# Optimization experiments

Hardware: AMD Instinct MI355X
Metric: run time of the kernel (lower is better)

The kernel has to match this reference:

```python
import jax, jax.numpy as jnp
import numpy as np


def setup_inputs() -> dict:
    key = jax.random.key(0)
    ks = jax.random.split(key, 12)
    B, T, S, D, A, E, L, V = 32, 64, 64, 1024, 512, 256, 1024, 12000
    s = 0.02  # weight scale for numerical stability
    return {
        "targets": jax.random.randint(ks[0], (B, T), 0, V),
        "options": jax.random.normal(ks[1], (B, S, D), jnp.float32),
        "h0": jax.random.normal(ks[2], (B, L), jnp.float32),
        "c0": jnp.zeros((B, L), jnp.float32),
        "emb": jax.random.normal(ks[3], (V, E), jnp.float32) * s,
        "W1": jax.random.normal(ks[4], (L, A), jnp.float32) * s,
        "b1": jnp.zeros((A,), jnp.float32),
        "W2": jax.random.normal(ks[5], (D, A), jnp.float32) * s,
        "b2": jnp.zeros((A,), jnp.float32),
        "Va": jax.random.normal(ks[6], (A, 1), jnp.float32) * s,
        "bVa": jnp.zeros((1,), jnp.float32),
        "Wx": jax.random.normal(ks[7], (D + E, 4 * L), jnp.float32) * s,
        "Wh": jax.random.normal(ks[8], (L, 4 * L), jnp.float32) * s,
        "bl": jnp.zeros((4 * L,), jnp.float32),
        "Wd": jax.random.normal(ks[9], (L, V), jnp.float32) * s,
        "bd": jnp.zeros((V,), jnp.float32),
    }


def reference(targets, options, h0, c0, emb, W1, b1, W2, b2, Va, bVa,
              Wx, Wh, bl, Wd, bd):
    L = h0.shape[-1]
    # W2(options) is step-invariant: hoist out of recurrent loop. [B,S,A]
    opt_proj = jnp.einsum('bsd,da->bsa', options, W2) + b2

    def step(carry, x_ids):
        h, c = carry
        # Bahdanau attention: score = V(tanh(W1(h) + W2(options)))
        score = jnp.tanh(h @ W1 + b1)[:, None, :] + opt_proj        # [B,S,A]
        score = jnp.einsum('bsa,ao->bso', score, Va) + bVa          # [B,S,1]
        w = jax.nn.softmax(score, axis=1)                           # [B,S,1]
        context = jnp.sum(w * options, axis=1)                      # [B,D]
        x = jnp.concatenate([context, emb[x_ids]], axis=-1)         # [B,D+E]
        # Keras LSTM cell, gate order i, f, g, o
        z = x @ Wx + h @ Wh + bl                                    # [B,4L]
        i, f, g, o = jnp.split(z, 4, axis=-1)
        c = jax.nn.sigmoid(f) * c + jax.nn.sigmoid(i) * jnp.tanh(g)
        h = jax.nn.sigmoid(o) * jnp.tanh(c)
        probs = jax.nn.softmax(h @ Wd + bd, axis=-1)                # [B,V]
        return (h, c), (probs, w[..., 0])

    (h, c), (out, attn) = jax.lax.scan(step, (h0, c0), targets.T)
    output = jnp.transpose(out, (1, 0, 2))   # [B,T,V]
    attention = attn[-1][..., None]          # last-step attention weights [B,S,1]
    return output, h, c, attention
```

## Files before the change

kernel.cpp:

```cpp
#include <hip/hip_runtime.h>
#include <math.h>


typedef _Float16 fp16;
typedef __attribute__((ext_vector_type(8))) _Float16 fp16x8;
typedef __attribute__((ext_vector_type(4))) _Float16 fp16x4;
typedef __attribute__((ext_vector_type(4))) float f32x4;

constexpr int B = 32, T = 64, S = 64, D = 1024, A = 512, E = 256, L = 1024, V = 12000;
constexpr int G = 4096;
constexpr size_t N_PROBS = (size_t)B * T * V;

__device__ inline void load_lds16(const void* g, void* l) {
  __builtin_amdgcn_global_load_lds(
      (const __attribute__((address_space(1))) unsigned int*)g,
      (__attribute__((address_space(3))) unsigned int*)l, 16, 0, 0);
}


__global__ void k_v2(const float* __restrict__ W2, const float* __restrict__ Va,
                     float* __restrict__ v2) {
  int gw = (blockIdx.x * blockDim.x + threadIdx.x) >> 6;
  int lane = threadIdx.x & 63;
  if (gw >= D) return;
  float acc = 0.f;
  for (int a = lane; a < A; a += 64) acc += W2[(size_t)gw * A + a] * Va[a];
  #pragma unroll
  for (int off = 32; off; off >>= 1) acc += __shfl_down(acc, off);
  if (lane == 0) v2[gw] = acc;
}

__global__ void k_score(const float* __restrict__ options, const float* __restrict__ v2,
                        float* __restrict__ w) {
  int row = (blockIdx.x * blockDim.x + threadIdx.x) >> 6;
  int lane = threadIdx.x & 63;
  if (row >= B * S) return;
  const float* orow = options + (size_t)row * D;
  float acc = 0.f;
  for (int d = lane; d < D; d += 64) acc += orow[d] * v2[d];
  #pragma unroll
  for (int off = 32; off; off >>= 1) acc += __shfl_down(acc, off);
  if (lane == 0) w[row] = acc;
}

__global__ __launch_bounds__(256) void k_attnctx(
    const float* __restrict__ options, const float* __restrict__ wat,
    float* __restrict__ oattn, float* __restrict__ ctx) {
  __shared__ float sw[64];
  const int b = blockIdx.x, tid = threadIdx.x;
  if (tid < 64) {
    float v = wat[b * 64 + tid];
    float m = v;
    #pragma unroll
    for (int off = 32; off; off >>= 1) m = fmaxf(m, __shfl_xor(m, off));
    float e = expf(v - m);
    float s = e;
    #pragma unroll
    for (int off = 32; off; off >>= 1) s += __shfl_xor(s, off);
    float res = e / s;
    sw[tid] = res;
    oattn[b * 64 + tid] = res;
  }
  __syncthreads();
  for (int d = tid; d < D; d += 256) {
    float acc = 0.f;
    #pragma unroll 8
    for (int s = 0; s < 64; ++s)
      acc += sw[s] * options[((size_t)(b * 64 + s)) * D + d];
    ctx[b * D + d] = acc;
  }
}

__global__ __launch_bounds__(256) void k_cx_part(
    const float* __restrict__ ctx, const float* __restrict__ Wx,
    float* __restrict__ cxp) {
  const int jt = blockIdx.x & 15;
  const int bg = (blockIdx.x >> 4) & 3;
  const int kc = blockIdx.x >> 6;
  const int j = jt * 256 + threadIdx.x;
  const int b0 = bg * 8, d0 = kc * 128;
  float acc[8];
  #pragma unroll
  for (int bb = 0; bb < 8; ++bb) acc[bb] = 0.f;
  for (int d = 0; d < 128; ++d) {
    float wv = Wx[(size_t)(d0 + d) * G + j];
    #pragma unroll
    for (int bb = 0; bb < 8; ++bb)
      acc[bb] = fmaf(ctx[(b0 + bb) * D + d0 + d], wv, acc[bb]);
  }
  #pragma unroll
  for (int bb = 0; bb < 8; ++bb)
    cxp[((size_t)kc * 32 + b0 + bb) * G + j] = acc[bb];
}

__global__ void k_cx_reduce(const float* __restrict__ cxp, const float* __restrict__ bl,
                            float* __restrict__ cx) {
  int i = blockIdx.x * 256 + threadIdx.x;
  float s = bl[i & 4095];
  #pragma unroll
  for (int kc = 0; kc < 8; ++kc) s += cxp[(size_t)kc * 131072 + i];
  cx[i] = s;
}

__global__ __launch_bounds__(256) void k_xform(
    const int* __restrict__ targets, const float* __restrict__ emb,
    const float* __restrict__ Wx, const float* __restrict__ Wh,
    const float* __restrict__ h0, const float* __restrict__ c0,
    fp16* __restrict__ eg, fp16* __restrict__ wx2t16, fp16* __restrict__ whp,
    fp16* __restrict__ h16, float* __restrict__ cst) {
  __shared__ float s[64][65];
  const int bid = blockIdx.x;
  const int tid = threadIdx.x;

  if (bid < 2048) {
    int tok = targets[bid];
    eg[(size_t)bid * E + tid] = (fp16)emb[(size_t)tok * E + tid];
    return;
  }
  if (bid < 2304) {
    const int lb = bid - 2048;
    const int et = lb >> 6, jt = lb & 63;
    const int e0 = et * 64, j0 = jt * 64;
    const int jj = tid & 63;
    #pragma unroll
    for (int k = 0; k < 16; ++k) {
      int ee = k * 4 + (tid >> 6);
      s[ee][jj] = Wx[(size_t)(D + e0 + ee) * G + j0 + jj];
    }
    __syncthreads();
    const int jc = tid >> 2, eq = tid & 3;
    fp16x8 o0, o1;
    #pragma unroll
    for (int i = 0; i < 8; ++i) {
      o0[i] = (fp16)s[eq * 16 + i][jc];
      o1[i] = (fp16)s[eq * 16 + 8 + i][jc];
    }
    size_t dst = (size_t)(j0 + jc) * E + e0 + eq * 16;
    *(fp16x8*)(wx2t16 + dst) = o0;
    *(fp16x8*)(wx2t16 + dst + 8) = o1;
    return;
  }
  if (bid < 3328) {
    const int lb = bid - 2304;
    const int lt = lb & 15, ct = lb >> 4;
    const int l0 = lt * 64, c0 = ct * 64;
    const int cc = tid & 63;
    #pragma unroll
    for (int k = 0; k < 16; ++k) {
      int ll = k * 4 + (tid >> 6);
      s[ll][cc] = Wh[(size_t)(l0 + ll) * G + c0 + cc];
    }
    __syncthreads();
    const int c = tid >> 2, lq = tid & 3;
    const int col = c0 + c, g = col >> 10, jj = col & 1023;
    const int rowp = ((jj >> 2) << 4) + (g << 2) + (jj & 3);
    fp16x8 o0, o1;
    #pragma unroll
    for (int i = 0; i < 8; ++i) {
      o0[i] = (fp16)s[lq * 16 + i][c];
      o1[i] = (fp16)s[lq * 16 + 8 + i][c];
    }
    size_t dst = (size_t)rowp * L + l0 + lq * 16;
    *(fp16x8*)(whp + dst) = o0;
    *(fp16x8*)(whp + dst + 8) = o1;
    return;
  }
  {
    const int lb = bid - 3328;
    int i = lb * 256 + tid;
    h16[i] = (fp16)h0[i];
    cst[i] = c0[i];
  }
}

__global__ __launch_bounds__(256) void k_pre_mfma(
    const fp16* __restrict__ Ag, const fp16* __restrict__ Bg,
    const float* __restrict__ cx, fp16* __restrict__ prep) {
  __shared__ __align__(16) char lds[32768];
  char* sA = lds;
  char* sB = lds + 16384;
  const int bid = blockIdx.x;
  const int swz = (bid & 7) * 64 + (bid >> 3);
  const int mt = swz >> 5, nt = swz & 31;
  const int m0 = mt * 128, n0 = nt * 128;
  const int tid = threadIdx.x, w = tid >> 6, lane = tid & 63;
  const int wr = w >> 1, wc = w & 1;

  f32x4 acc[4][4];
  #pragma unroll
  for (int i = 0; i < 4; ++i)
    #pragma unroll
    for (int j = 0; j < 4; ++j) acc[i][j] = (f32x4){0.f, 0.f, 0.f, 0.f};

  int rowc[4], sloc[4];
  #pragma unroll
  for (int i = 0; i < 4; ++i) {
    int c = i * 4 + w;
    rowc[i] = c * 8 + (lane >> 3);
    sloc[i] = (lane & 7) ^ (rowc[i] & 7);
  }

  for (int kk = 0; kk < 4; ++kk) {
    if (kk) __syncthreads();
    const char* ga = (const char*)Ag + kk * 128;
    const char* gb = (const char*)Bg + kk * 128;
    #pragma unroll
    for (int i = 0; i < 4; ++i) {
      int c = i * 4 + w;
      load_lds16(ga + (size_t)(m0 + rowc[i]) * 512 + sloc[i] * 16, sA + c * 1024);
      load_lds16(gb + (size_t)(n0 + rowc[i]) * 512 + sloc[i] * 16, sB + c * 1024);
    }
    __syncthreads();
    #pragma unroll
    for (int ks = 0; ks < 2; ++ks) {
      fp16x8 av[4], bv[4];
      #pragma unroll
      for (int f = 0; f < 4; ++f) {
        int ra = wr * 64 + f * 16 + (lane & 15);
        int ca = (ks * 4 + (lane >> 4)) ^ (ra & 7);
        av[f] = *(const fp16x8*)(sA + ra * 128 + ca * 16);
        int rb = wc * 64 + f * 16 + (lane & 15);
        int cb = (ks * 4 + (lane >> 4)) ^ (rb & 7);
        bv[f] = *(const fp16x8*)(sB + rb * 128 + cb * 16);
      }
      #pragma unroll
      for (int fm = 0; fm < 4; ++fm)
        #pragma unroll
        for (int fn = 0; fn < 4; ++fn)
          acc[fm][fn] = __builtin_amdgcn_mfma_f32_16x16x32_f16(
              av[fm], bv[fn], acc[fm][fn], 0, 0, 0);
    }
  }

  const int r0o = m0 + wr * 64 + ((lane >> 4) << 2);
  const int c0o = n0 + wc * 64 + (lane & 15);
  #pragma unroll
  for (int fn = 0; fn < 4; ++fn) {
    int colg = c0o + fn * 16;
    int g = colg >> 10, jj = colg & 1023;
    int jb = jj >> 2, jo = jj & 3;
    #pragma unroll
    for (int fm = 0; fm < 4; ++fm) {
      #pragma unroll
      for (int r = 0; r < 4; ++r) {
        int row = r0o + fm * 16 + r;
        int b = row >> 6, t = row & 63;
        float v = acc[fm][fn][r] + cx[(size_t)b * G + colg];
        prep[(((size_t)t * 256 + jb) * 32 + b) * 16 + jo * 4 + g] = (fp16)v;
      }
    }
  }
}

__global__ __launch_bounds__(512) void k_step4(
    const fp16* __restrict__ Whp, const fp16* __restrict__ prep,
    const fp16* __restrict__ hin, fp16* __restrict__ hout,
    float* __restrict__ cst, fp16* __restrict__ Hb16,
    float* __restrict__ out_h, float* __restrict__ out_c, int t) {
  __shared__ float zred[8 * 2 * 64 * 4];
  __shared__ float zf[32][16];
  const int jb = blockIdx.x;
  const int tid = threadIdx.x;
  const int w = tid >> 6, lane = tid & 63;
  const int fr = lane & 15, kc = lane >> 4;

  float pf[4];
  float cprev = 0.f;
  const int gb = tid >> 2, gjo = tid & 3, gj = jb * 4 + gjo;
  if (tid < 128) {
    fp16x4 pv = *(const fp16x4*)(prep + (((size_t)t * 256 + jb) * 32 + gb) * 16 + gjo * 4);
    #pragma unroll
    for (int g = 0; g < 4; ++g) pf[g] = (float)pv[g];
    cprev = cst[gb * 1024 + gj];
  }

  f32x4 acc[2];
  acc[0] = (f32x4){0.f, 0.f, 0.f, 0.f};
  acc[1] = (f32x4){0.f, 0.f, 0.f, 0.f};
  const fp16* bb = Whp + (size_t)(jb * 16 + fr) * L;
  #pragma unroll
  for (int kk = 0; kk < 4; ++kk) {
    const int k0 = (w * 4 + kk) * 32 + kc * 8;
    fp16x8 bv = *(const fp16x8*)(bb + k0);
    #pragma unroll
    for (int m = 0; m < 2; ++m) {
      fp16x8 av = *(const fp16x8*)(hin + (size_t)(m * 16 + fr) * L + k0);
      acc[m] = __builtin_amdgcn_mfma_f32_16x16x32_f16(av, bv, acc[m], 0, 0, 0);
    }
  }
  #pragma unroll
  for (int m = 0; m < 2; ++m)
    *(f32x4*)&zred[((w * 2 + m) * 64 + lane) * 4] = acc[m];
  __syncthreads();
  {
    const int b = tid >> 4, c = tid & 15;
    const int lane2 = (((b & 15) >> 2) << 4) | c;
    const int reg = b & 3, m = b >> 4;
    float s = 0.f;
    #pragma unroll
    for (int ww = 0; ww < 8; ++ww)
      s += zred[((ww * 2 + m) * 64 + lane2) * 4 + reg];
    zf[b][c] = s;
  }
  __syncthreads();
  if (tid < 128) {
    float zi = zf[gb][gjo] + pf[0];
    float zff = zf[gb][4 + gjo] + pf[1];
    float zg = zf[gb][8 + gjo] + pf[2];
    float zo = zf[gb][12 + gjo] + pf[3];
    float si = 1.f / (1.f + expf(-zi));
    float sf = 1.f / (1.f + expf(-zff));
    float tg = tanhf(zg);
    float so = 1.f / (1.f + expf(-zo));
    float cn = sf * cprev + si * tg;
    float hn = so * tanhf(cn);
    const int hi_idx = gb * 1024 + gj;
    cst[hi_idx] = cn;
    hout[hi_idx] = (fp16)hn;
    Hb16[(size_t)(gb * 64 + t) * L + gj] = (fp16)hn;
    if (t == T - 1) {
      out_h[hi_idx] = hn;
      out_c[hi_idx] = cn;
    }
  }
}

__global__ __launch_bounds__(256) void k_wdt(const float* __restrict__ Wd,
                                             fp16* __restrict__ Wdt) {
  __shared__ float s[64][65];
  const int lt = blockIdx.x & 15;
  const int vt = blockIdx.x >> 4;
  const int l0 = lt * 64, v0 = vt * 64;
  const int tid = threadIdx.x;
  const int lv = tid & 63;
  #pragma unroll
  for (int k = 0; k < 16; ++k) {
    int ll = k * 4 + (tid >> 6);
    int v = v0 + lv;
    s[ll][lv] = (v < V) ? Wd[(size_t)(l0 + ll) * V + v] : 0.f;
  }
  __syncthreads();
  const int vv = tid >> 2, lq = tid & 3;
  fp16x8 o0, o1;
  #pragma unroll
  for (int j = 0; j < 8; ++j) {
    o0[j] = (fp16)s[lq * 16 + j][vv];
    o1[j] = (fp16)s[lq * 16 + 8 + j][vv];
  }
  fp16* dst = Wdt + (size_t)(v0 + vv) * 1024 + l0 + lq * 16;
  *(fp16x8*)dst = o0;
  *(fp16x8*)(dst + 8) = o1;
}

__global__ __launch_bounds__(256) void k_logits_mfma(
    const fp16* __restrict__ Ag, const fp16* __restrict__ Btg,
    const float* __restrict__ bd, float* __restrict__ out) {
  __shared__ __align__(16) char lds[32768];
  char* sA = lds;
  char* sB = lds + 16384;
  const int bid = blockIdx.x;
  const int wg = (bid & 7) * 188 + (bid >> 3);
  const int nt = wg >> 4, mt = wg & 15;
  const int m0 = mt * 128, n0 = nt * 128;
  const int tid = threadIdx.x, w = tid >> 6, lane = tid & 63;
  const int wr = w >> 1, wc = w & 1;

  f32x4 acc[4][4];
  #pragma unroll
  for (int i = 0; i < 4; ++i)
    #pragma unroll
    for (int j = 0; j < 4; ++j) acc[i][j] = (f32x4){0.f, 0.f, 0.f, 0.f};

  int rowc[4], sloc[4];
  #pragma unroll
  for (int i = 0; i < 4; ++i) {
    int c = i * 4 + w;
    rowc[i] = c * 8 + (lane >> 3);
    sloc[i] = (lane & 7) ^ (rowc[i] & 7);
  }

  for (int kk = 0; kk < 16; ++kk) {
    if (kk) __syncthreads();
    const char* ga = (const char*)Ag + kk * 128;
    const char* gb = (const char*)Btg + kk * 128;
    #pragma unroll
    for (int i = 0; i < 4; ++i) {
      int c = i * 4 + w;
      load_lds16(ga + (size_t)(m0 + rowc[i]) * 2048 + sloc[i] * 16, sA + c * 1024);
      load_lds16(gb + (size_t)(n0 + rowc[i]) * 2048 + sloc[i] * 16, sB + c * 1024);
    }
    __syncthreads();
    #pragma unroll
    for (int ks = 0; ks < 2; ++ks) {
      fp16x8 av[4], bv[4];
      #pragma unroll
      for (int f = 0; f < 4; ++f) {
        int ra = wr * 64 + f * 16 + (lane & 15);
        int ca = (ks * 4 + (lane >> 4)) ^ (ra & 7);
        av[f] = *(const fp16x8*)(sA + ra * 128 + ca * 16);
        int rb = wc * 64 + f * 16 + (lane & 15);
        int cb = (ks * 4 + (lane >> 4)) ^ (rb & 7);
        bv[f] = *(const fp16x8*)(sB + rb * 128 + cb * 16);
      }
      #pragma unroll
      for (int fm = 0; fm < 4; ++fm)
        #pragma unroll
        for (int fn = 0; fn < 4; ++fn)
          acc[fm][fn] = __builtin_amdgcn_mfma_f32_16x16x32_f16(
              av[fm], bv[fn], acc[fm][fn], 0, 0, 0);
    }
  }

  float* ctile = (float*)lds;
  float bvv[4];
  #pragma unroll
  for (int fn = 0; fn < 4; ++fn) {
    int colg = n0 + wc * 64 + fn * 16 + (lane & 15);
    bvv[fn] = (colg < V) ? bd[colg] : 0.f;
  }
  #pragma unroll
  for (int p = 0; p < 2; ++p) {
    __syncthreads();
    if (wr == p) {
      const int col = wc * 64 + (lane & 15);
      #pragma unroll
      for (int fn = 0; fn < 4; ++fn) {
        #pragma unroll
        for (int fm = 0; fm < 4; ++fm) {
          int row = fm * 16 + ((lane >> 4) << 2);
          #pragma unroll
          for (int r = 0; r < 4; ++r)
            ctile[(row + r) * 128 + col + fn * 16] = acc[fm][fn][r] + bvv[fn];
        }
      }
    }
    __syncthreads();
    #pragma unroll
    for (int it = 0; it < 8; ++it) {
      int idx = it * 256 + tid;
      int row = idx >> 5, ch = idx & 31;
      int colg = n0 + ch * 4;
      if (colg < V)
        *(float4*)&out[(size_t)(m0 + p * 64 + row) * V + colg] =
            *(float4*)&ctile[row * 128 + ch * 4];
    }
  }
}

__global__ __launch_bounds__(256) void k_softmax(float* __restrict__ logits) {
  __shared__ float sred[4];
  float* row = logits + (size_t)blockIdx.x * V;
  const int tid = threadIdx.x;
  const float4* rv = (const float4*)row;
  float4 v[12];
  float m = -3.4e38f;
  #pragma unroll
  for (int k = 0; k < 12; ++k) {
    int i = tid + k * 256;
    if (i < 3000) {
      v[k] = rv[i];
      m = fmaxf(fmaxf(m, fmaxf(v[k].x, v[k].y)), fmaxf(v[k].z, v[k].w));
    }
  }
  #pragma unroll
  for (int off = 32; off; off >>= 1) m = fmaxf(m, __shfl_xor(m, off));
  if ((tid & 63) == 0) sred[tid >> 6] = m;
  __syncthreads();
  const float M = fmaxf(fmaxf(sred[0], sred[1]), fmaxf(sred[2], sred[3]));
  float s = 0.f;
  #pragma unroll
  for (int k = 0; k < 12; ++k) {
    int i = tid + k * 256;
    if (i < 3000) {
      v[k].x = __expf(v[k].x - M); v[k].y = __expf(v[k].y - M);
      v[k].z = __expf(v[k].z - M); v[k].w = __expf(v[k].w - M);
      s += v[k].x + v[k].y + v[k].z + v[k].w;
    }
  }
  #pragma unroll
  for (int off = 32; off; off >>= 1) s += __shfl_xor(s, off);
  __syncthreads();
  if ((tid & 63) == 0) sred[tid >> 6] = s;
  __syncthreads();
  const float inv = 1.f / (sred[0] + sred[1] + sred[2] + sred[3]);
  float4* ov = (float4*)row;
  #pragma unroll
  for (int k = 0; k < 12; ++k) {
    int i = tid + k * 256;
    if (i < 3000) {
      float4 x = v[k];
      x.x *= inv; x.y *= inv; x.z *= inv; x.w *= inv;
      ov[i] = x;
    }
  }
}


extern "C" void kernel_launch(void* const* d_in, const int* in_sizes, int n_in,
                              void* d_out, int out_size, void* d_ws, size_t ws_size,
                              hipStream_t stream) {
  const int*   targets = (const int*)d_in[0];
  const float* options = (const float*)d_in[1];
  const float* h0      = (const float*)d_in[2];
  const float* c0      = (const float*)d_in[3];
  const float* emb     = (const float*)d_in[4];
  const float* W2      = (const float*)d_in[7];
  const float* Va      = (const float*)d_in[9];
  const float* Wx      = (const float*)d_in[11];
  const float* Wh      = (const float*)d_in[12];
  const float* bl      = (const float*)d_in[13];
  const float* Wd      = (const float*)d_in[14];
  const float* bd      = (const float*)d_in[15];

  float* out      = (float*)d_out;
  float* out_h    = out + N_PROBS;
  float* out_c    = out_h + (size_t)B * L;
  float* out_attn = out_c + (size_t)B * L;

  char* wsb = (char*)d_ws;
  float* v2     = (float*)(wsb);
  float* wat    = (float*)(wsb + 4096);
  float* ctx    = (float*)(wsb + 12288);
  float* cx     = (float*)(wsb + 143360);
  float* cst    = (float*)(wsb + 667648);
  fp16*  hA     = (fp16*)(wsb + 798720);
  fp16*  hB     = (fp16*)(wsb + 864256);
  fp16*  Eg16   = (fp16*)(wsb + 1191936);
  fp16*  Wx2t16 = (fp16*)(wsb + 2240512);
  fp16*  Hb16   = (fp16*)(wsb + 1191936);
  fp16*  Whp    = (fp16*)(wsb + 7483392);
  fp16*  prep   = (fp16*)(wsb + 15872000);
  float* cxp    = (float*)(wsb + 15872000);
  fp16*  Wdt    = (fp16*)(wsb + 7483392);

  k_v2<<<256, 256, 0, stream>>>(W2, Va, v2);
  k_score<<<512, 256, 0, stream>>>(options, v2, wat);
  k_attnctx<<<32, 256, 0, stream>>>(options, wat, out_attn, ctx);
  k_cx_part<<<512, 256, 0, stream>>>(ctx, Wx, cxp);
  k_cx_reduce<<<512, 256, 0, stream>>>(cxp, bl, cx);

  k_xform<<<3456, 256, 0, stream>>>(targets, emb, Wx, Wh, h0, c0,
                                    Eg16, Wx2t16, Whp, hA, cst);

  k_pre_mfma<<<512, 256, 0, stream>>>(Eg16, Wx2t16, cx, prep);

  for (int t = 0; t < T; ++t) {
    const fp16* hin = (t & 1) ? hB : hA;
    fp16* hout = (t & 1) ? hA : hB;
    k_step4<<<256, 512, 0, stream>>>(Whp, prep, hin, hout, cst, Hb16,
                                     out_h, out_c, t);
  }

  k_wdt<<<188 * 16, 256, 0, stream>>>(Wd, Wdt);
  k_logits_mfma<<<1504, 256, 0, stream>>>(Hb16, Wdt, bd, out);
  k_softmax<<<B * T, 256, 0, stream>>>(out);
}
```

Baseline: 541.2 us.

## Fuse attention score kernels into one and fold context projection into transform kernel

```diff
diff --git a/kernel.cpp b/kernel.cpp
--- a/kernel.cpp
+++ b/kernel.cpp
@@ -17,39 +17,51 @@
       (__attribute__((address_space(3))) unsigned int*)l, 16, 0, 0);
 }
 
-
-__global__ void k_v2(const float* __restrict__ W2, const float* __restrict__ Va,
-                     float* __restrict__ v2) {
-  int gw = (blockIdx.x * blockDim.x + threadIdx.x) >> 6;
-  int lane = threadIdx.x & 63;
-  if (gw >= D) return;
-  float acc = 0.f;
-  for (int a = lane; a < A; a += 64) acc += W2[(size_t)gw * A + a] * Va[a];
-  #pragma unroll
-  for (int off = 32; off; off >>= 1) acc += __shfl_down(acc, off);
-  if (lane == 0) v2[gw] = acc;
-}
-
-__global__ void k_score(const float* __restrict__ options, const float* __restrict__ v2,
-                        float* __restrict__ w) {
-  int row = (blockIdx.x * blockDim.x + threadIdx.x) >> 6;
-  int lane = threadIdx.x & 63;
-  if (row >= B * S) return;
-  const float* orow = options + (size_t)row * D;
-  float acc = 0.f;
-  for (int d = lane; d < D; d += 64) acc += orow[d] * v2[d];
-  #pragma unroll
-  for (int off = 32; off; off >>= 1) acc += __shfl_down(acc, off);
-  if (lane == 0) w[row] = acc;
-}
-
-__global__ __launch_bounds__(256) void k_attnctx(
-    const float* __restrict__ options, const float* __restrict__ wat,
-    float* __restrict__ oattn, float* __restrict__ ctx) {
+__global__ __launch_bounds__(256) void k_attn(
+    const float* __restrict__ W2, const float* __restrict__ Va,
+    const float* __restrict__ options, float* __restrict__ oattn,
+    float* __restrict__ ctx) {
+  __shared__ float sv2[1024];
   __shared__ float sw[64];
   const int b = blockIdx.x, tid = threadIdx.x;
+  const int wv = tid >> 6, lane = tid & 63;
+
+  float vva[8];
+  #pragma unroll
+  for (int k = 0; k < 8; ++k) vva[k] = Va[lane + k * 64];
+  for (int r = 0; r < 256; r += 2) {
+    const int d0 = wv * 256 + r, d1 = d0 + 1;
+    const float* w0 = W2 + (size_t)d0 * A;
+    const float* w1 = W2 + (size_t)d1 * A;
+    float a0 = 0.f, a1 = 0.f;
+    #pragma unroll
+    for (int k = 0; k < 8; ++k) {
+      a0 += w0[lane + k * 64] * vva[k];
+      a1 += w1[lane + k * 64] * vva[k];
+    }
+    #pragma unroll
+    for (int off = 32; off; off >>= 1) {
+      a0 += __shfl_down(a0, off);
+      a1 += __shfl_down(a1, off);
+    }
+    if (lane == 0) { sv2[d0] = a0; sv2[d1] = a1; }
+  }
+  __syncthreads();
+
+  for (int r = 0; r < 16; ++r) {
+    const int s = wv * 16 + r;
+    const float* orow = options + ((size_t)b * 64 + s) * D;
+    float acc = 0.f;
+    #pragma unroll
+    for (int k = 0; k < 16; ++k) acc += orow[lane + k * 64] * sv2[lane + k * 64];
+    #pragma unroll
+    for (int off = 32; off; off >>= 1) acc += __shfl_down(acc, off);
+    if (lane == 0) sw[s] = acc;
+  }
+  __syncthreads();
+
   if (tid < 64) {
-    float v = wat[b * 64 + tid];
+    float v = sw[tid];
     float m = v;
     #pragma unroll
     for (int off = 32; off; off >>= 1) m = fmaxf(m, __shfl_xor(m, off));
@@ -62,6 +74,7 @@
     oattn[b * 64 + tid] = res;
   }
   __syncthreads();
+
   for (int d = tid; d < D; d += 256) {
     float acc = 0.f;
     #pragma unroll 8
@@ -71,28 +84,6 @@
   }
 }
 
-__global__ __launch_bounds__(256) void k_cx_part(
-    const float* __restrict__ ctx, const float* __restrict__ Wx,
-    float* __restrict__ cxp) {
-  const int jt = blockIdx.x & 15;
-  const int bg = (blockIdx.x >> 4) & 3;
-  const int kc = blockIdx.x >> 6;
-  const int j = jt * 256 + threadIdx.x;
-  const int b0 = bg * 8, d0 = kc * 128;
-  float acc[8];
-  #pragma unroll
-  for (int bb = 0; bb < 8; ++bb) acc[bb] = 0.f;
-  for (int d = 0; d < 128; ++d) {
-    float wv = Wx[(size_t)(d0 + d) * G + j];
-    #pragma unroll
-    for (int bb = 0; bb < 8; ++bb)
-      acc[bb] = fmaf(ctx[(b0 + bb) * D + d0 + d], wv, acc[bb]);
-  }
-  #pragma unroll
-  for (int bb = 0; bb < 8; ++bb)
-    cxp[((size_t)kc * 32 + b0 + bb) * G + j] = acc[bb];
-}
-
 __global__ void k_cx_reduce(const float* __restrict__ cxp, const float* __restrict__ bl,
                             float* __restrict__ cx) {
   int i = blockIdx.x * 256 + threadIdx.x;
@@ -106,8 +97,9 @@
     const int* __restrict__ targets, const float* __restrict__ emb,
     const float* __restrict__ Wx, const float* __restrict__ Wh,
     const float* __restrict__ h0, const float* __restrict__ c0,
+    const float* __restrict__ ctx,
     fp16* __restrict__ eg, fp16* __restrict__ wx2t16, fp16* __restrict__ whp,
-    fp16* __restrict__ h16, float* __restrict__ cst) {
+    fp16* __restrict__ h16, float* __restrict__ cst, float* __restrict__ cxp) {
   __shared__ float s[64][65];
   const int bid = blockIdx.x;
   const int tid = threadIdx.x;
@@ -143,16 +135,16 @@
   if (bid < 3328) {
     const int lb = bid - 2304;
     const int lt = lb & 15, ct = lb >> 4;
-    const int l0 = lt * 64, c0 = ct * 64;
+    const int l0 = lt * 64, c0w = ct * 64;
     const int cc = tid & 63;
     #pragma unroll
     for (int k = 0; k < 16; ++k) {
       int ll = k * 4 + (tid >> 6);
-      s[ll][cc] = Wh[(size_t)(l0 + ll) * G + c0 + cc];
+      s[ll][cc] = Wh[(size_t)(l0 + ll) * G + c0w + cc];
     }
     __syncthreads();
     const int c = tid >> 2, lq = tid & 3;
-    const int col = c0 + c, g = col >> 10, jj = col & 1023;
+    const int col = c0w + c, g = col >> 10, jj = col & 1023;
     const int rowp = ((jj >> 2) << 4) + (g << 2) + (jj & 3);
     fp16x8 o0, o1;
     #pragma unroll
@@ -165,11 +157,32 @@
     *(fp16x8*)(whp + dst + 8) = o1;
     return;
   }
-  {
+  if (bid < 3456) {
     const int lb = bid - 3328;
     int i = lb * 256 + tid;
     h16[i] = (fp16)h0[i];
     cst[i] = c0[i];
+    return;
+  }
+  {
+    const int lb = bid - 3456;
+    const int jt = lb & 15;
+    const int bg = (lb >> 4) & 3;
+    const int kc = lb >> 6;
+    const int j = jt * 256 + tid;
+    const int b0 = bg * 8, d0 = kc * 128;
+    float acc[8];
+    #pragma unroll
+    for (int bb = 0; bb < 8; ++bb) acc[bb] = 0.f;
+    for (int d = 0; d < 128; ++d) {
+      float wv = Wx[(size_t)(d0 + d) * G + j];
+      #pragma unroll
+      for (int bb = 0; bb < 8; ++bb)
+        acc[bb] = fmaf(ctx[(b0 + bb) * D + d0 + d], wv, acc[bb]);
+    }
+    #pragma unroll
+    for (int bb = 0; bb < 8; ++bb)
+      cxp[((size_t)kc * 32 + b0 + bb) * G + j] = acc[bb];
   }
 }
 
@@ -518,8 +531,6 @@
   float* out_attn = out_c + (size_t)B * L;
 
   char* wsb = (char*)d_ws;
-  float* v2     = (float*)(wsb);
-  float* wat    = (float*)(wsb + 4096);
   float* ctx    = (float*)(wsb + 12288);
   float* cx     = (float*)(wsb + 143360);
   float* cst    = (float*)(wsb + 667648);
@@ -533,14 +544,11 @@
   float* cxp    = (float*)(wsb + 15872000);
   fp16*  Wdt    = (fp16*)(wsb + 7483392);
 
-  k_v2<<<256, 256, 0, stream>>>(W2, Va, v2);
-  k_score<<<512, 256, 0, stream>>>(options, v2, wat);
-  k_attnctx<<<32, 256, 0, stream>>>(options, wat, out_attn, ctx);
-  k_cx_part<<<512, 256, 0, stream>>>(ctx, Wx, cxp);
+  k_attn<<<32, 256, 0, stream>>>(W2, Va, options, out_attn, ctx);
+
+  k_xform<<<3968, 256, 0, stream>>>(targets, emb, Wx, Wh, h0, c0, ctx,
+                                    Eg16, Wx2t16, Whp, hA, cst, cxp);
   k_cx_reduce<<<512, 256, 0, stream>>>(cxp, bl, cx);
-
-  k_xform<<<3456, 256, 0, stream>>>(targets, emb, Wx, Wh, h0, c0,
-                                    Eg16, Wx2t16, Whp, hA, cst);
 
   k_pre_mfma<<<512, 256, 0, stream>>>(Eg16, Wx2t16, cx, prep);
 
```

Result: slower. 593.4 us (+9.6%).
